# Performance work log

Measured on AMD Instinct MI355X. Metric: run time of the kernel, lower is better.

Reference implementation:

```python
import jax, jax.numpy as jnp
from jax import lax
import numpy as np

B, T, H31, W = 16, 96, 31, 64
C1, C2, LH, NC = 16, 32, 64, 10

def _conv(x, w, b):
    # NCHW conv, 3x3, padding=1 ('SAME'), fused bias + relu
    y = lax.conv_general_dilated(x, w, (1, 1), 'SAME', dimension_numbers=('NCHW', 'OIHW', 'NCHW'))
    return jax.nn.relu(y + b[None, :, None, None])

def _lstm(xs, w_ih, w_hh, b):
    # xs: [T, B, D]; PyTorch gate order i, f, g, o
    Hd = w_hh.shape[1]
    def step(carry, x):
        h, c = carry
        g = x @ w_ih.T + h @ w_hh.T + b
        i, f, gg, o = jnp.split(g, 4, -1)
        c = jax.nn.sigmoid(f) * c + jax.nn.sigmoid(i) * jnp.tanh(gg)
        h = jax.nn.sigmoid(o) * jnp.tanh(c)
        return (h, c), h
    z = jnp.zeros((xs.shape[1], Hd), xs.dtype)
    _, hs = lax.scan(step, (z, z), xs)
    return hs  # [T, B, H]

def setup_inputs():
    key = jax.random.key(0)
    ks = jax.random.split(key, 26)
    n = lambda i, shape, s=0.1: jax.random.normal(ks[i], shape, jnp.float32) * s
    return {
        'x_real': jax.random.normal(ks[0], (B, T, H31, W), jnp.float32),
        'x_imag': jax.random.normal(ks[1], (B, T, H31, W), jnp.float32),
        'lengths': jax.random.randint(ks[2], (B,), 1, T + 1),
        'conv1r_w': n(3, (C1, 1, 3, 3), 0.3), 'conv1r_b': n(4, (C1,)),
        'conv1i_w': n(5, (C1, 1, 3, 3), 0.3), 'conv1i_b': n(6, (C1,)),
        'conv2r_w': n(7, (C2, C1, 3, 3), 0.15), 'conv2r_b': n(8, (C2,)),
        'conv2i_w': n(9, (C2, C1, 3, 3), 0.15), 'conv2i_b': n(10, (C2,)),
        'fus_w': n(11, (2 * C2, 4 * C2), 0.1), 'fus_b': n(12, (2 * C2,)),
        'wf_ih': n(13, (4 * LH, 2 * C2), 0.1), 'wf_hh': n(14, (4 * LH, LH), 0.1),
        'bf_ih': n(15, (4 * LH,)), 'bf_hh': n(16, (4 * LH,)),
        'wb_ih': n(17, (4 * LH, 2 * C2), 0.1), 'wb_hh': n(18, (4 * LH, LH), 0.1),
        'bb_ih': n(19, (4 * LH,)), 'bb_hh': n(20, (4 * LH,)),
        'fc_w': n(21, (NC, 2 * LH), 0.1), 'fc_b': n(22, (NC,)),
    }

def reference(x_real, x_imag, lengths, conv1r_w, conv1r_b, conv1i_w, conv1i_b, conv2r_w, conv2r_b, conv2i_w, conv2i_b, fus_w, fus_b, wf_ih, wf_hh, bf_ih, bf_hh, wb_ih, wb_hh, bb_ih, bb_hh, fc_w, fc_b):
    Bb, Tt, Hh, Ww = x_real.shape
    # batch all (sample, timestep) conv work together: [B*T, 1, 31, W]
    xr = x_real.reshape(Bb * Tt, 1, Hh, Ww)
    xi = x_imag.reshape(Bb * Tt, 1, Hh, Ww)
    rf = _conv(_conv(xr, conv1r_w, conv1r_b), conv2r_w, conv2r_b)
    mf = _conv(_conv(xi, conv1i_w, conv1i_b), conv2i_w, conv2i_b)
    r = rf.mean((-2, -1))  # AdaptiveAvgPool2d((1,1)) -> [B*T, C2]
    m = mf.mean((-2, -1))
    mag = jnp.sqrt(r * r + m * m)           # abs(r + 1j*m)
    ang = jnp.arctan2(m, r)                 # angle(r + 1j*m)
    feat = jnp.concatenate([r, m, mag, ang], -1)  # [B*T, 4*C2]
    fused = jax.nn.relu(feat @ fus_w.T + fus_b).reshape(Bb, Tt, -1)  # dropout = identity (eval)
    # forward LSTM: output at t < length is unaffected by padded steps
    hs_f = _lstm(fused.transpose(1, 0, 2), wf_ih, wf_hh, bf_ih + bf_hh)  # [T, B, LH]
    last_f = hs_f[lengths - 1, jnp.arange(Bb)]
    # backward LSTM over length-reversed sequence (packed-sequence semantics)
    rev_idx = jnp.clip(lengths[:, None] - 1 - jnp.arange(Tt)[None, :], 0, Tt - 1)  # [B, T]
    x_rev = jnp.take_along_axis(fused, rev_idx[:, :, None], axis=1)
    hs_b = _lstm(x_rev.transpose(1, 0, 2), wb_ih, wb_hh, bb_ih + bb_hh)
    # backward hidden at original position length-1 is the first reverse step
    last = jnp.concatenate([last_f, hs_b[0]], -1)  # [B, 2*LH]
    return last @ fc_w.T + fc_b
```

## Files before the change

kernel.cpp:

```cpp
#include <hip/hip_runtime.h>
#include <math.h>

#define BB 16
#define TT 96
#define HH 31
#define WW 64
#define BT (BB*TT)
#define C1 16
#define C2 32
#define LH 64
#define NC 10

typedef _Float16 half8 __attribute__((ext_vector_type(8)));
typedef float floatx16 __attribute__((ext_vector_type(16)));

#define XPAD 66
#define YPAD 33
#define NPOS (YPAD*XPAD)
#define SXBYTES (NPOS*32 + 128)

__device__ __forceinline__ int swz(int byte) {
    return byte ^ (((byte >> 7) & 7) << 4);
}

__global__ __launch_bounds__(512, 4)
void conv_pool_mfma(const float* __restrict__ xr, const float* __restrict__ xi,
                    const float* __restrict__ w1r, const float* __restrict__ b1r,
                    const float* __restrict__ w1i, const float* __restrict__ b1i,
                    const float* __restrict__ w2r, const float* __restrict__ b2r,
                    const float* __restrict__ w2i, const float* __restrict__ b2i,
                    float* __restrict__ pool_r, float* __restrict__ pool_m)
{
    __shared__ __align__(128) unsigned char s_x[SXBYTES];
    __shared__ float s_pool[C2];

    const int tid  = threadIdx.x;
    const int lane = tid & 63;
    const int img  = blockIdx.x;
    const int part = blockIdx.y;

    const float* xg = (part ? xi : xr) + img*(HH*WW);
    const float* w1 = part ? w1i : w1r;
    const float* b1 = part ? b1i : b1r;
    const float* w2 = part ? w2i : w2r;
    const float* b2 = part ? b2i : b2r;
    float* poolo = (part ? pool_m : pool_r) + img*C2;

    for (int i = tid*16; i < SXBYTES; i += 512*16)
        *reinterpret_cast<int4*>(s_x + i) = make_int4(0,0,0,0);
    if (tid < C2) s_pool[tid] = 0.f;
    __syncthreads();

    if (tid < HH*16) {
        const int y  = tid >> 4;
        const int x0 = (tid & 15) << 2;
        float patch[3][6];
        #pragma unroll
        for (int ky = 0; ky < 3; ++ky) {
            int row = y + ky - 1;
            #pragma unroll
            for (int j = 0; j < 6; ++j) {
                int col = x0 + j - 1;
                patch[ky][j] = (row >= 0 && row < HH && col >= 0 && col < WW)
                                 ? xg[row*WW + col] : 0.f;
            }
        }
        float acc[16][4];
        #pragma unroll
        for (int ch = 0; ch < 16; ++ch) {
            float bb = b1[ch];
            #pragma unroll
            for (int j = 0; j < 4; ++j) acc[ch][j] = bb;
        }
        #pragma unroll
        for (int ky = 0; ky < 3; ++ky)
            #pragma unroll
            for (int kx = 0; kx < 3; ++kx) {
                #pragma unroll
                for (int ch = 0; ch < 16; ++ch) {
                    float wv = w1[ch*9 + ky*3 + kx];
                    #pragma unroll
                    for (int j = 0; j < 4; ++j)
                        acc[ch][j] += patch[ky][kx + j] * wv;
                }
            }
        #pragma unroll
        for (int j = 0; j < 4; ++j) {
            half8 lo, hi;
            #pragma unroll
            for (int ch = 0; ch < 8; ++ch) {
                lo[ch] = (_Float16)fmaxf(acc[ch][j],     0.f);
                hi[ch] = (_Float16)fmaxf(acc[8+ch][j],   0.f);
            }
            int pos = (y + 1)*XPAD + (x0 + j + 1);
            *reinterpret_cast<half8*>(s_x + swz(pos*32))      = lo;
            *reinterpret_cast<half8*>(s_x + swz(pos*32 + 16)) = hi;
        }
    }

    const int oc  = lane & 31;
    const int icb = (lane >> 5) * 8;
    half8 af[9];
    #pragma unroll
    for (int t = 0; t < 9; ++t) {
        half8 v;
        #pragma unroll
        for (int i = 0; i < 8; ++i)
            v[i] = (_Float16)w2[(oc*C1 + icb + i)*9 + t];
        af[t] = v;
    }
    float bias[16];
    #pragma unroll
    for (int r = 0; r < 16; ++r)
        bias[r] = b2[(r & 3) + 8*(r >> 2) + 4*(lane >> 5)];

    __syncthreads();

    float pool[16];
    #pragma unroll
    for (int r = 0; r < 16; ++r) pool[r] = 0.f;

    const int wav = tid >> 6;
    const int halfoff = (lane >> 5) << 4;
    for (int tile = wav; tile < 62; tile += 8) {
        int y  = tile >> 1;
        int x0 = (tile & 1) * 32;
        floatx16 acc;
        #pragma unroll
        for (int r = 0; r < 16; ++r) acc[r] = bias[r];
        int pbase = y*XPAD + x0 + (lane & 31);
        #pragma unroll
        for (int ky = 0; ky < 3; ++ky) {
            #pragma unroll
            for (int kx = 0; kx < 3; ++kx) {
                int pos = pbase + ky*XPAD + kx;
                half8 b = *reinterpret_cast<const half8*>(s_x + swz(pos*32 + halfoff));
                acc = __builtin_amdgcn_mfma_f32_32x32x16_f16(af[ky*3+kx], b, acc, 0, 0, 0);
            }
        }
        #pragma unroll
        for (int r = 0; r < 16; ++r) pool[r] += fmaxf(acc[r], 0.f);
    }

    #pragma unroll
    for (int m = 1; m <= 16; m <<= 1) {
        #pragma unroll
        for (int r = 0; r < 16; ++r) pool[r] += __shfl_xor(pool[r], m, 64);
    }
    if ((lane & 31) == 0) {
        #pragma unroll
        for (int r = 0; r < 16; ++r)
            atomicAdd(&s_pool[(r & 3) + 8*(r >> 2) + 4*(lane >> 5)], pool[r]);
    }
    __syncthreads();
    if (tid < C2) poolo[tid] = s_pool[tid] * (1.f/1984.f);
}

__global__ __launch_bounds__(256)
void feat_fused_kernel(const float* __restrict__ pool_r, const float* __restrict__ pool_m,
                       const float* __restrict__ fus_w, const float* __restrict__ fus_b,
                       float* __restrict__ fused)
{
    __shared__ __align__(16) float s_feat[4][128];
    int tid = threadIdx.x;
    int n0 = blockIdx.x * 4;
    if (tid < 128) {
        int s = tid >> 5, c = tid & 31;
        float r = pool_r[(n0+s)*C2 + c];
        float m = pool_m[(n0+s)*C2 + c];
        s_feat[s][c]      = r;
        s_feat[s][32 + c] = m;
        s_feat[s][64 + c] = sqrtf(r*r + m*m);
        s_feat[s][96 + c] = atan2f(m, r);
    }
    __syncthreads();
    int s = tid >> 6, k = tid & 63;
    float acc = fus_b[k];
    const float4* wv = reinterpret_cast<const float4*>(fus_w + k*128);
    const float4* fv = reinterpret_cast<const float4*>(&s_feat[s][0]);
    #pragma unroll
    for (int j = 0; j < 32; ++j) {
        float4 w = wv[j], f = fv[j];
        acc += w.x*f.x + w.y*f.y + w.z*f.z + w.w*f.w;
    }
    fused[(n0+s)*64 + k] = fmaxf(acc, 0.f);
}

__device__ __forceinline__ float sigm(float x){ return 1.f/(1.f + __expf(-x)); }
__device__ __forceinline__ float ftanh(float x){
    float xc = fminf(fmaxf(x, -15.f), 15.f);
    float e = __expf(2.f*xc);
    return (e - 1.f)/(e + 1.f);
}

__global__ __launch_bounds__(256, 1)
void lstm_kernel(const float* __restrict__ fused, const int* __restrict__ lengths,
                 const float* __restrict__ wf_ih, const float* __restrict__ wf_hh,
                 const float* __restrict__ bf_ih, const float* __restrict__ bf_hh,
                 const float* __restrict__ wb_ih, const float* __restrict__ wb_hh,
                 const float* __restrict__ bb_ih, const float* __restrict__ bb_hh,
                 float* __restrict__ last_f, float* __restrict__ hb0)
{
    __shared__ float s_x[64], s_h[64], s_g[256];
    const int g = threadIdx.x;
    const int b = blockIdx.x & 15;
    const bool bwd = blockIdx.x >= 16;
    const int len = lengths[b];

    if (!bwd) {
        float wih[64], whh[64];
        const float* wi = wf_ih + g*64;
        const float* wh = wf_hh + g*64;
        #pragma unroll
        for (int j = 0; j < 64; j += 4) {
            float4 a = *reinterpret_cast<const float4*>(wi + j);
            wih[j]=a.x; wih[j+1]=a.y; wih[j+2]=a.z; wih[j+3]=a.w;
            float4 c = *reinterpret_cast<const float4*>(wh + j);
            whh[j]=c.x; whh[j+1]=c.y; whh[j+2]=c.z; whh[j+3]=c.w;
        }
        const float bg = bf_ih[g] + bf_hh[g];
        float creg = 0.f;
        if (g < 64) { s_h[g] = 0.f; s_x[g] = fused[(b*TT)*64 + g]; }
        __syncthreads();
        for (int t = 0; t < TT; ++t) {
            float a0=0.f, a1=0.f, a2=0.f, a3=0.f;
            #pragma unroll
            for (int j = 0; j < 64; j += 4) {
                a0 += s_x[j]  *wih[j];   a1 += s_x[j+1]*wih[j+1];
                a2 += s_x[j+2]*wih[j+2]; a3 += s_x[j+3]*wih[j+3];
            }
            #pragma unroll
            for (int j = 0; j < 64; j += 4) {
                a0 += s_h[j]  *whh[j];   a1 += s_h[j+1]*whh[j+1];
                a2 += s_h[j+2]*whh[j+2]; a3 += s_h[j+3]*whh[j+3];
            }
            s_g[g] = (a0+a1) + (a2+a3) + bg;
            __syncthreads();
            if (g < 64) {
                float iv = sigm(s_g[g]);
                float fv = sigm(s_g[64+g]);
                float gv = ftanh(s_g[128+g]);
                float ov = sigm(s_g[192+g]);
                creg = fv*creg + iv*gv;
                float h = ov*ftanh(creg);
                s_h[g] = h;
                if (t == len-1) last_f[b*64+g] = h;
                if (t+1 < TT) s_x[g] = fused[(b*TT + t+1)*64 + g];
            }
            __syncthreads();
        }
    } else {
        float wih[64];
        const float* wi = wb_ih + g*64;
        #pragma unroll
        for (int j = 0; j < 64; j += 4) {
            float4 a = *reinterpret_cast<const float4*>(wi + j);
            wih[j]=a.x; wih[j+1]=a.y; wih[j+2]=a.z; wih[j+3]=a.w;
        }
        const float bg = bb_ih[g] + bb_hh[g];
        if (g < 64) s_x[g] = fused[(b*TT + (len-1))*64 + g];
        __syncthreads();
        float a0=0.f, a1=0.f, a2=0.f, a3=0.f;
        #pragma unroll
        for (int j = 0; j < 64; j += 4) {
            a0 += s_x[j]  *wih[j];   a1 += s_x[j+1]*wih[j+1];
            a2 += s_x[j+2]*wih[j+2]; a3 += s_x[j+3]*wih[j+3];
        }
        s_g[g] = (a0+a1) + (a2+a3) + bg;
        __syncthreads();
        if (g < 64) {
            float iv = sigm(s_g[g]);
            float gv = ftanh(s_g[128+g]);
            float ov = sigm(s_g[192+g]);
            float c = iv*gv;
            float h = ov*ftanh(c);
            hb0[b*64+g] = h;
        }
    }
}

__global__ __launch_bounds__(256)
void final_fc_kernel(const float* __restrict__ last_f, const float* __restrict__ hb0,
                     const float* __restrict__ fc_w, const float* __restrict__ fc_b,
                     float* __restrict__ out)
{
    int t = threadIdx.x;
    if (t >= BB*NC) return;
    int b = t / NC, k = t % NC;
    float acc = fc_b[k];
    const float* w = fc_w + k*128;
    #pragma unroll
    for (int j = 0; j < 64; ++j) acc += last_f[b*64+j]*w[j];
    #pragma unroll
    for (int j = 0; j < 64; ++j) acc += hb0[b*64+j]*w[64+j];
    out[b*NC + k] = acc;
}

extern "C" void kernel_launch(void* const* d_in, const int* in_sizes, int n_in,
                              void* d_out, int out_size, void* d_ws, size_t ws_size,
                              hipStream_t stream)
{
    const float* x_real = (const float*)d_in[0];
    const float* x_imag = (const float*)d_in[1];
    const int*   lengths= (const int*)d_in[2];
    const float* c1r_w = (const float*)d_in[3];
    const float* c1r_b = (const float*)d_in[4];
    const float* c1i_w = (const float*)d_in[5];
    const float* c1i_b = (const float*)d_in[6];
    const float* c2r_w = (const float*)d_in[7];
    const float* c2r_b = (const float*)d_in[8];
    const float* c2i_w = (const float*)d_in[9];
    const float* c2i_b = (const float*)d_in[10];
    const float* fus_w = (const float*)d_in[11];
    const float* fus_b = (const float*)d_in[12];
    const float* wf_ih = (const float*)d_in[13];
    const float* wf_hh = (const float*)d_in[14];
    const float* bf_ih = (const float*)d_in[15];
    const float* bf_hh = (const float*)d_in[16];
    const float* wb_ih = (const float*)d_in[17];
    const float* wb_hh = (const float*)d_in[18];
    const float* bb_ih = (const float*)d_in[19];
    const float* bb_hh = (const float*)d_in[20];
    const float* fc_w  = (const float*)d_in[21];
    const float* fc_b  = (const float*)d_in[22];
    float* out = (float*)d_out;

    float* ws     = (float*)d_ws;
    float* pool_r = ws;
    float* pool_m = pool_r + BT*C2;
    float* fusedb = pool_m + BT*C2;
    float* last_f = fusedb + BT*64;
    float* hb0    = last_f + BB*64;

    conv_pool_mfma<<<dim3(BT, 2), 512, 0, stream>>>(
        x_real, x_imag, c1r_w, c1r_b, c1i_w, c1i_b,
        c2r_w, c2r_b, c2i_w, c2i_b, pool_r, pool_m);

    feat_fused_kernel<<<BT/4, 256, 0, stream>>>(pool_r, pool_m, fus_w, fus_b, fusedb);

    lstm_kernel<<<32, 256, 0, stream>>>(fusedb, lengths,
        wf_ih, wf_hh, bf_ih, bf_hh, wb_ih, wb_hh, bb_ih, bb_hh, last_f, hb0);

    final_fc_kernel<<<1, 256, 0, stream>>>(last_f, hb0, fc_w, fc_b, out);
}
```

Before: 357.4 us.

## Fuse feature projection into LSTM, precompute input gates, trim conv zeroing

Merges the feature/fusion-linear kernel into the LSTM kernel and precomputes all input-to-gate projections for every timestep in shared memory before the recurrence, leaving only the hidden-state matvec on the serial path. The backward branch computes only the single timestep it needs. The conv kernel zeroes only the padding border instead of the whole shared buffer, splits conv1 into two 8-channel passes to cut register pressure, reorders conv2 LDS loads ahead of the MFMAs, and lowers the occupancy hint. It removes one launch and a global round trip, but adds a large shared-memory footprint and serial precompute work in the LSTM blocks.

```diff
diff --git a/kernel.cpp b/kernel.cpp
--- a/kernel.cpp
+++ b/kernel.cpp
@@ -23,7 +23,7 @@
     return byte ^ (((byte >> 7) & 7) << 4);
 }
 
-__global__ __launch_bounds__(512, 4)
+__global__ __launch_bounds__(512, 2)
 void conv_pool_mfma(const float* __restrict__ xr, const float* __restrict__ xi,
                     const float* __restrict__ w1r, const float* __restrict__ b1r,
                     const float* __restrict__ w1i, const float* __restrict__ b1i,
@@ -46,10 +46,19 @@
     const float* b2 = part ? b2i : b2r;
     float* poolo = (part ? pool_m : pool_r) + img*C2;
 
-    for (int i = tid*16; i < SXBYTES; i += 512*16)
-        *reinterpret_cast<int4*>(s_x + i) = make_int4(0,0,0,0);
     if (tid < C2) s_pool[tid] = 0.f;
-    __syncthreads();
+
+    if (tid < 194) {
+        int pos;
+        if (tid < 66)       pos = tid;
+        else if (tid < 132) pos = 32*XPAD + (tid - 66);
+        else {
+            int i = tid - 132;
+            pos = (1 + (i >> 1))*XPAD + ((i & 1) ? 65 : 0);
+        }
+        *reinterpret_cast<int4*>(s_x + swz(pos*32))      = make_int4(0,0,0,0);
+        *reinterpret_cast<int4*>(s_x + swz(pos*32 + 16)) = make_int4(0,0,0,0);
+    }
 
     if (tid < HH*16) {
         const int y  = tid >> 4;
@@ -65,36 +74,36 @@
                                  ? xg[row*WW + col] : 0.f;
             }
         }
-        float acc[16][4];
-        #pragma unroll
-        for (int ch = 0; ch < 16; ++ch) {
-            float bb = b1[ch];
-            #pragma unroll
-            for (int j = 0; j < 4; ++j) acc[ch][j] = bb;
-        }
-        #pragma unroll
-        for (int ky = 0; ky < 3; ++ky)
-            #pragma unroll
-            for (int kx = 0; kx < 3; ++kx) {
-                #pragma unroll
-                for (int ch = 0; ch < 16; ++ch) {
-                    float wv = w1[ch*9 + ky*3 + kx];
+        #pragma unroll
+        for (int p = 0; p < 2; ++p) {
+            float acc[8][4];
+            #pragma unroll
+            for (int ch = 0; ch < 8; ++ch) {
+                float bb = b1[p*8 + ch];
+                #pragma unroll
+                for (int j = 0; j < 4; ++j) acc[ch][j] = bb;
+            }
+            #pragma unroll
+            for (int ky = 0; ky < 3; ++ky)
+                #pragma unroll
+                for (int kx = 0; kx < 3; ++kx) {
                     #pragma unroll
-                    for (int j = 0; j < 4; ++j)
-                        acc[ch][j] += patch[ky][kx + j] * wv;
+                    for (int ch = 0; ch < 8; ++ch) {
+                        float wv = w1[(p*8 + ch)*9 + ky*3 + kx];
+                        #pragma unroll
+                        for (int j = 0; j < 4; ++j)
+                            acc[ch][j] += patch[ky][kx + j] * wv;
+                    }
                 }
-            }
-        #pragma unroll
-        for (int j = 0; j < 4; ++j) {
-            half8 lo, hi;
-            #pragma unroll
-            for (int ch = 0; ch < 8; ++ch) {
-                lo[ch] = (_Float16)fmaxf(acc[ch][j],     0.f);
-                hi[ch] = (_Float16)fmaxf(acc[8+ch][j],   0.f);
-            }
-            int pos = (y + 1)*XPAD + (x0 + j + 1);
-            *reinterpret_cast<half8*>(s_x + swz(pos*32))      = lo;
-            *reinterpret_cast<half8*>(s_x + swz(pos*32 + 16)) = hi;
+            #pragma unroll
+            for (int j = 0; j < 4; ++j) {
+                half8 v;
+                #pragma unroll
+                for (int ch = 0; ch < 8; ++ch)
+                    v[ch] = (_Float16)fmaxf(acc[ch][j], 0.f);
+                int pos = (y + 1)*XPAD + (x0 + j + 1);
+                *reinterpret_cast<half8*>(s_x + swz(pos*32 + p*16)) = v;
+            }
         }
     }
 
@@ -122,25 +131,37 @@
 
     const int wav = tid >> 6;
     const int halfoff = (lane >> 5) << 4;
+
+    #define LDB(dst, ky, kx) do { \
+        int byte_ = (pbase + (ky)*XPAD + (kx))*32 + halfoff; \
+        dst = *reinterpret_cast<const half8*>(s_x + swz(byte_)); } while (0)
+
     for (int tile = wav; tile < 62; tile += 8) {
         int y  = tile >> 1;
         int x0 = (tile & 1) * 32;
+        int pbase = y*XPAD + x0 + (lane & 31);
         floatx16 acc;
         #pragma unroll
         for (int r = 0; r < 16; ++r) acc[r] = bias[r];
-        int pbase = y*XPAD + x0 + (lane & 31);
-        #pragma unroll
-        for (int ky = 0; ky < 3; ++ky) {
-            #pragma unroll
-            for (int kx = 0; kx < 3; ++kx) {
-                int pos = pbase + ky*XPAD + kx;
-                half8 b = *reinterpret_cast<const half8*>(s_x + swz(pos*32 + halfoff));
-                acc = __builtin_amdgcn_mfma_f32_32x32x16_f16(af[ky*3+kx], b, acc, 0, 0, 0);
-            }
-        }
+
+        half8 r0a, r0b, r0c, r1a, r1b, r1c, r2a, r2b, r2c;
+        LDB(r0a, 0, 0); LDB(r0b, 0, 1); LDB(r0c, 0, 2);
+        LDB(r1a, 1, 0); LDB(r1b, 1, 1); LDB(r1c, 1, 2);
+        acc = __builtin_amdgcn_mfma_f32_32x32x16_f16(af[0], r0a, acc, 0, 0, 0);
+        acc = __builtin_amdgcn_mfma_f32_32x32x16_f16(af[1], r0b, acc, 0, 0, 0);
+        acc = __builtin_amdgcn_mfma_f32_32x32x16_f16(af[2], r0c, acc, 0, 0, 0);
+        LDB(r2a, 2, 0); LDB(r2b, 2, 1); LDB(r2c, 2, 2);
+        acc = __builtin_amdgcn_mfma_f32_32x32x16_f16(af[3], r1a, acc, 0, 0, 0);
+        acc = __builtin_amdgcn_mfma_f32_32x32x16_f16(af[4], r1b, acc, 0, 0, 0);
+        acc = __builtin_amdgcn_mfma_f32_32x32x16_f16(af[5], r1c, acc, 0, 0, 0);
+        acc = __builtin_amdgcn_mfma_f32_32x32x16_f16(af[6], r2a, acc, 0, 0, 0);
+        acc = __builtin_amdgcn_mfma_f32_32x32x16_f16(af[7], r2b, acc, 0, 0, 0);
+        acc = __builtin_amdgcn_mfma_f32_32x32x16_f16(af[8], r2c, acc, 0, 0, 0);
+
         #pragma unroll
         for (int r = 0; r < 16; ++r) pool[r] += fmaxf(acc[r], 0.f);
     }
+    #undef LDB
 
     #pragma unroll
     for (int m = 1; m <= 16; m <<= 1) {
@@ -154,36 +175,6 @@
     }
     __syncthreads();
     if (tid < C2) poolo[tid] = s_pool[tid] * (1.f/1984.f);
-}
-
-__global__ __launch_bounds__(256)
-void feat_fused_kernel(const float* __restrict__ pool_r, const float* __restrict__ pool_m,
-                       const float* __restrict__ fus_w, const float* __restrict__ fus_b,
-                       float* __restrict__ fused)
-{
-    __shared__ __align__(16) float s_feat[4][128];
-    int tid = threadIdx.x;
-    int n0 = blockIdx.x * 4;
-    if (tid < 128) {
-        int s = tid >> 5, c = tid & 31;
-        float r = pool_r[(n0+s)*C2 + c];
-        float m = pool_m[(n0+s)*C2 + c];
-        s_feat[s][c]      = r;
-        s_feat[s][32 + c] = m;
-        s_feat[s][64 + c] = sqrtf(r*r + m*m);
-        s_feat[s][96 + c] = atan2f(m, r);
-    }
-    __syncthreads();
-    int s = tid >> 6, k = tid & 63;
-    float acc = fus_b[k];
-    const float4* wv = reinterpret_cast<const float4*>(fus_w + k*128);
-    const float4* fv = reinterpret_cast<const float4*>(&s_feat[s][0]);
-    #pragma unroll
-    for (int j = 0; j < 32; ++j) {
-        float4 w = wv[j], f = fv[j];
-        acc += w.x*f.x + w.y*f.y + w.z*f.z + w.w*f.w;
-    }
-    fused[(n0+s)*64 + k] = fmaxf(acc, 0.f);
 }
 
 __device__ __forceinline__ float sigm(float x){ return 1.f/(1.f + __expf(-x)); }
@@ -193,88 +184,160 @@
     return (e - 1.f)/(e + 1.f);
 }
 
-__global__ __launch_bounds__(256, 1)
-void lstm_kernel(const float* __restrict__ fused, const int* __restrict__ lengths,
-                 const float* __restrict__ wf_ih, const float* __restrict__ wf_hh,
-                 const float* __restrict__ bf_ih, const float* __restrict__ bf_hh,
-                 const float* __restrict__ wb_ih, const float* __restrict__ wb_hh,
-                 const float* __restrict__ bb_ih, const float* __restrict__ bb_hh,
-                 float* __restrict__ last_f, float* __restrict__ hb0)
+__global__ __launch_bounds__(512, 1)
+void lstm_fused(const float* __restrict__ pool_r, const float* __restrict__ pool_m,
+                const int* __restrict__ lengths,
+                const float* __restrict__ fus_w, const float* __restrict__ fus_b,
+                const float* __restrict__ wf_ih, const float* __restrict__ wf_hh,
+                const float* __restrict__ bf_ih, const float* __restrict__ bf_hh,
+                const float* __restrict__ wb_ih, const float* __restrict__ wb_hh,
+                const float* __restrict__ bb_ih, const float* __restrict__ bb_hh,
+                float* __restrict__ last_f, float* __restrict__ hb0)
 {
-    __shared__ float s_x[64], s_h[64], s_g[256];
-    const int g = threadIdx.x;
-    const int b = blockIdx.x & 15;
+    __shared__ __align__(16) float s_gx[TT*256];
+    __shared__ __align__(16) float s_fused[TT][64];
+    __shared__ float s_h[64];
+    __shared__ float s_g[256];
+
+    const int tid = threadIdx.x;
+    const int b   = blockIdx.x & 15;
     const bool bwd = blockIdx.x >= 16;
     const int len = lengths[b];
 
     if (!bwd) {
-        float wih[64], whh[64];
-        const float* wi = wf_ih + g*64;
-        const float* wh = wf_hh + g*64;
-        #pragma unroll
-        for (int j = 0; j < 64; j += 4) {
-            float4 a = *reinterpret_cast<const float4*>(wi + j);
-            wih[j]=a.x; wih[j+1]=a.y; wih[j+2]=a.z; wih[j+3]=a.w;
-            float4 c = *reinterpret_cast<const float4*>(wh + j);
-            whh[j]=c.x; whh[j+1]=c.y; whh[j+2]=c.z; whh[j+3]=c.w;
-        }
-        const float bg = bf_ih[g] + bf_hh[g];
+        for (int i = tid; i < TT*32; i += 512) {
+            int t = i >> 5, c = i & 31;
+            float r = pool_r[(b*TT + t)*C2 + c];
+            float m = pool_m[(b*TT + t)*C2 + c];
+            float* f = s_gx + t*128;
+            f[c]      = r;
+            f[32 + c] = m;
+            f[64 + c] = sqrtf(r*r + m*m);
+            f[96 + c] = atan2f(m, r);
+        }
+        __syncthreads();
+
+        {
+            const int k = tid & 63, tq = tid >> 6;
+            float4 wreg[32];
+            #pragma unroll
+            for (int q = 0; q < 32; ++q)
+                wreg[q] = *reinterpret_cast<const float4*>(fus_w + k*128 + q*4);
+            const float bk = fus_b[k];
+            for (int j = 0; j < 12; ++j) {
+                int t = tq*12 + j;
+                const float* f = s_gx + t*128;
+                float a0=0.f, a1=0.f, a2=0.f, a3=0.f;
+                #pragma unroll
+                for (int q = 0; q < 32; ++q) {
+                    float4 fv = *reinterpret_cast<const float4*>(f + q*4);
+                    a0 += wreg[q].x*fv.x; a1 += wreg[q].y*fv.y;
+                    a2 += wreg[q].z*fv.z; a3 += wreg[q].w*fv.w;
+                }
+                s_fused[t][k] = fmaxf((a0+a1) + (a2+a3) + bk, 0.f);
+            }
+        }
+        __syncthreads();
+
+        {
+            const int g = tid & 255, th = tid >> 8;
+            float wih[64];
+            #pragma unroll
+            for (int q = 0; q < 64; q += 4) {
+                float4 a = *reinterpret_cast<const float4*>(wf_ih + g*64 + q);
+                wih[q]=a.x; wih[q+1]=a.y; wih[q+2]=a.z; wih[q+3]=a.w;
+            }
+            const float bg = bf_ih[g] + bf_hh[g];
+            for (int j = 0; j < 48; ++j) {
+                int t = th*48 + j;
+                float a0=0.f, a1=0.f, a2=0.f, a3=0.f;
+                #pragma unroll
+                for (int q = 0; q < 64; q += 4) {
+                    float4 fv = *reinterpret_cast<const float4*>(&s_fused[t][q]);
+                    a0 += wih[q]*fv.x;   a1 += wih[q+1]*fv.y;
+                    a2 += wih[q+2]*fv.z; a3 += wih[q+3]*fv.w;
+                }
+                s_gx[t*256 + g] = (a0+a1) + (a2+a3) + bg;
+            }
+        }
+        __syncthreads();
+
+        const int g = tid & 255;
+        float whh[64];
+        #pragma unroll
+        for (int q = 0; q < 64; q += 4) {
+            float4 a = *reinterpret_cast<const float4*>(wf_hh + g*64 + q);
+            whh[q]=a.x; whh[q+1]=a.y; whh[q+2]=a.z; whh[q+3]=a.w;
+        }
+        if (tid < 64) s_h[tid] = 0.f;
+        __syncthreads();
         float creg = 0.f;
-        if (g < 64) { s_h[g] = 0.f; s_x[g] = fused[(b*TT)*64 + g]; }
-        __syncthreads();
         for (int t = 0; t < TT; ++t) {
-            float a0=0.f, a1=0.f, a2=0.f, a3=0.f;
-            #pragma unroll
-            for (int j = 0; j < 64; j += 4) {
-                a0 += s_x[j]  *wih[j];   a1 += s_x[j+1]*wih[j+1];
-                a2 += s_x[j+2]*wih[j+2]; a3 += s_x[j+3]*wih[j+3];
-            }
-            #pragma unroll
-            for (int j = 0; j < 64; j += 4) {
-                a0 += s_h[j]  *whh[j];   a1 += s_h[j+1]*whh[j+1];
-                a2 += s_h[j+2]*whh[j+2]; a3 += s_h[j+3]*whh[j+3];
-            }
-            s_g[g] = (a0+a1) + (a2+a3) + bg;
+            if (tid < 256) {
+                float a0=0.f, a1=0.f, a2=0.f, a3=0.f;
+                #pragma unroll
+                for (int q = 0; q < 64; q += 4) {
+                    float4 hv = *reinterpret_cast<const float4*>(&s_h[q]);
+                    a0 += whh[q]*hv.x;   a1 += whh[q+1]*hv.y;
+                    a2 += whh[q+2]*hv.z; a3 += whh[q+3]*hv.w;
+                }
+                s_g[g] = (a0+a1) + (a2+a3) + s_gx[t*256 + g];
+            }
             __syncthreads();
-            if (g < 64) {
-                float iv = sigm(s_g[g]);
-                float fv = sigm(s_g[64+g]);
-                float gv = ftanh(s_g[128+g]);
-                float ov = sigm(s_g[192+g]);
+            if (tid < 64) {
+                float iv = sigm(s_g[tid]);
+                float fv = sigm(s_g[64+tid]);
+                float gv = ftanh(s_g[128+tid]);
+                float ov = sigm(s_g[192+tid]);
                 creg = fv*creg + iv*gv;
                 float h = ov*ftanh(creg);
-                s_h[g] = h;
-                if (t == len-1) last_f[b*64+g] = h;
-                if (t+1 < TT) s_x[g] = fused[(b*TT + t+1)*64 + g];
+                s_h[tid] = h;
+                if (t == len-1) last_f[b*64+tid] = h;
             }
             __syncthreads();
         }
     } else {
-        float wih[64];
-        const float* wi = wb_ih + g*64;
-        #pragma unroll
-        for (int j = 0; j < 64; j += 4) {
-            float4 a = *reinterpret_cast<const float4*>(wi + j);
-            wih[j]=a.x; wih[j+1]=a.y; wih[j+2]=a.z; wih[j+3]=a.w;
-        }
-        const float bg = bb_ih[g] + bb_hh[g];
-        if (g < 64) s_x[g] = fused[(b*TT + (len-1))*64 + g];
-        __syncthreads();
-        float a0=0.f, a1=0.f, a2=0.f, a3=0.f;
-        #pragma unroll
-        for (int j = 0; j < 64; j += 4) {
-            a0 += s_x[j]  *wih[j];   a1 += s_x[j+1]*wih[j+1];
-            a2 += s_x[j+2]*wih[j+2]; a3 += s_x[j+3]*wih[j+3];
-        }
-        s_g[g] = (a0+a1) + (a2+a3) + bg;
-        __syncthreads();
-        if (g < 64) {
-            float iv = sigm(s_g[g]);
-            float gv = ftanh(s_g[128+g]);
-            float ov = sigm(s_g[192+g]);
+        const int t0 = len - 1;
+        if (tid < 32) {
+            int c = tid;
+            float r = pool_r[(b*TT + t0)*C2 + c];
+            float m = pool_m[(b*TT + t0)*C2 + c];
+            s_gx[c]      = r;
+            s_gx[32 + c] = m;
+            s_gx[64 + c] = sqrtf(r*r + m*m);
+            s_gx[96 + c] = atan2f(m, r);
+        }
+        __syncthreads();
+        if (tid < 64) {
+            float acc = fus_b[tid];
+            const float4* wv = reinterpret_cast<const float4*>(fus_w + tid*128);
+            #pragma unroll
+            for (int q = 0; q < 32; ++q) {
+                float4 w = wv[q];
+                float4 f = *reinterpret_cast<const float4*>(s_gx + q*4);
+                acc += w.x*f.x + w.y*f.y + w.z*f.z + w.w*f.w;
+            }
+            s_fused[0][tid] = fmaxf(acc, 0.f);
+        }
+        __syncthreads();
+        if (tid < 256) {
+            float acc = bb_ih[tid] + bb_hh[tid];
+            const float4* wv = reinterpret_cast<const float4*>(wb_ih + tid*64);
+            #pragma unroll
+            for (int q = 0; q < 16; ++q) {
+                float4 w = wv[q];
+                float4 f = *reinterpret_cast<const float4*>(&s_fused[0][q*4]);
+                acc += w.x*f.x + w.y*f.y + w.z*f.z + w.w*f.w;
+            }
+            s_g[tid] = acc;
+        }
+        __syncthreads();
+        if (tid < 64) {
+            float iv = sigm(s_g[tid]);
+            float gv = ftanh(s_g[128+tid]);
+            float ov = sigm(s_g[192+tid]);
             float c = iv*gv;
-            float h = ov*ftanh(c);
-            hb0[b*64+g] = h;
+            hb0[b*64+tid] = ov*ftanh(c);
         }
     }
 }
@@ -328,18 +391,16 @@
     float* ws     = (float*)d_ws;
     float* pool_r = ws;
     float* pool_m = pool_r + BT*C2;
-    float* fusedb = pool_m + BT*C2;
-    float* last_f = fusedb + BT*64;
-    float* hb0    = last_f + BB*64;
+    float* last_f = pool_m + BT*C2;
+    float* hb0    = last_f + BB*LH;
 
     conv_pool_mfma<<<dim3(BT, 2), 512, 0, stream>>>(
         x_real, x_imag, c1r_w, c1r_b, c1i_w, c1i_b,
         c2r_w, c2r_b, c2i_w, c2i_b, pool_r, pool_m);
 
-    feat_fused_kernel<<<BT/4, 256, 0, stream>>>(pool_r, pool_m, fus_w, fus_b, fusedb);
-
-    lstm_kernel<<<32, 256, 0, stream>>>(fusedb, lengths,
-        wf_ih, wf_hh, bf_ih, bf_hh, wb_ih, wb_hh, bb_ih, bb_hh, last_f, hb0);
+    lstm_fused<<<32, 512, 0, stream>>>(pool_r, pool_m, lengths,
+        fus_w, fus_b, wf_ih, wf_hh, bf_ih, bf_hh,
+        wb_ih, wb_hh, bb_ih, bb_hh, last_f, hb0);
 
     final_fc_kernel<<<1, 256, 0, stream>>>(last_f, hb0, fc_w, fc_b, out);
 }
```

Measured after the change: 347.4 us. 2.8% less time.
